# Performance work log

Measured on AMD Instinct MI355X. Metric: run time of the kernel, lower is better.

Reference implementation:

```python
import jax, jax.numpy as jnp
import numpy as np

N = 100000
E = 3200000
NFEAT = 512
NHID = 256
NCLASS = 40


def setup_inputs() -> dict:
    key = jax.random.key(0)
    k1, k2, k3, k4, k5 = jax.random.split(key, 5)
    x = jax.random.normal(k1, (N, NFEAT), dtype=jnp.float32)
    edge_index = jax.random.randint(k2, (2, E), 0, N, dtype=jnp.int64)
    edge_weight = jax.random.uniform(k3, (E,), dtype=jnp.float32)
    W1 = jax.random.normal(k4, (NFEAT, NHID), dtype=jnp.float32) / np.sqrt(NFEAT)
    b1 = jnp.zeros((NHID,), dtype=jnp.float32)
    W2 = jax.random.normal(k5, (NHID, NCLASS), dtype=jnp.float32) / np.sqrt(NHID)
    b2 = jnp.zeros((NCLASS,), dtype=jnp.float32)
    return {"x": x, "edge_index": edge_index, "edge_weight": edge_weight,
            "W1": W1, "b1": b1, "W2": W2, "b2": b2}


def reference(x, edge_index, edge_weight, W1, b1, W2, b2):
    rows = edge_index[0]  # destination nodes
    cols = edge_index[1]  # source nodes

    def spmm(h):
        # adj @ h via edge-list gather -> weight -> scatter-add  [N, d]
        return jax.ops.segment_sum(edge_weight[:, None] * h[cols], rows,
                                   num_segments=N)

    # baseline == 1 path of GCN.forward (dropout is identity in eval)
    h = jax.nn.relu(spmm(x @ W1 + b1))               # [N, NHID]
    logits = spmm(h @ W2 + b2)                       # [N, NCLASS]
    # original computes t.log(F.softmax(x, dim=1))
    return jnp.log(jax.nn.softmax(logits, axis=1))
```

## Files before the change

### kernel.cpp

```cpp
#include <hip/hip_runtime.h>
#include <hip/hip_fp16.h>
#include <math.h>

#define NNODES 100000
#define NEDGES 3200000
#define NFEAT  512
#define NHID   256
#define NCLASS 40
#define DPB    128
#define NBUCK  782
#define TILE   16384
#define NTILE  196

typedef _Float16 half8 __attribute__((ext_vector_type(8)));
typedef _Float16 half4 __attribute__((ext_vector_type(4)));
typedef float  f32x4  __attribute__((ext_vector_type(4)));

__global__ __launch_bounds__(256) void w1_f16_kernel(
    const float* __restrict__ W1, _Float16* __restrict__ W1T)
{
    const int i = blockIdx.x * 256 + threadIdx.x;
    if (i >= NFEAT * NHID) return;
    const int k = i >> 8;
    const int n = i & 255;
    W1T[n * NFEAT + k] = (_Float16)W1[i];
}

__global__ __launch_bounds__(256) void gemm1_f16_kernel(
    const float* __restrict__ x, const _Float16* __restrict__ Bt,
    const float* __restrict__ b1, _Float16* __restrict__ h0)
{
    __shared__ __align__(16) _Float16 As[64 * 40];
    const int t = threadIdx.x;
    const int lane = t & 63;
    const int w = t >> 6;
    const int row0 = blockIdx.x * 64;
    const int wn0 = w * 64;
    const int fr = lane & 15;
    const int fq = lane >> 4;
    const int srow = t >> 2;
    const int skq  = (t & 3) * 8;
    const int grow = row0 + srow;
    const float* xp = x + (size_t)grow * NFEAT + skq;
    _Float16* ap = &As[srow * 40 + skq];

    f32x4 acc[4][4] = {};

    for (int k0 = 0; k0 < NFEAT; k0 += 32) {
        half8 hv;
        if (grow < NNODES) {
            const float4 u0 = *(const float4*)(xp + k0);
            const float4 u1 = *(const float4*)(xp + k0 + 4);
            hv[0] = (_Float16)u0.x; hv[1] = (_Float16)u0.y;
            hv[2] = (_Float16)u0.z; hv[3] = (_Float16)u0.w;
            hv[4] = (_Float16)u1.x; hv[5] = (_Float16)u1.y;
            hv[6] = (_Float16)u1.z; hv[7] = (_Float16)u1.w;
        } else {
            #pragma unroll
            for (int j = 0; j < 8; ++j) hv[j] = (_Float16)0.f;
        }
        __syncthreads();
        *(half8*)ap = hv;
        __syncthreads();

        half8 a_f[4];
        #pragma unroll
        for (int mt = 0; mt < 4; ++mt)
            a_f[mt] = *(const half8*)&As[(mt * 16 + fr) * 40 + fq * 8];
        half8 b_f[4];
        #pragma unroll
        for (int nt = 0; nt < 4; ++nt) {
            const int n = wn0 + nt * 16 + fr;
            b_f[nt] = *(const half8*)(Bt + (size_t)n * NFEAT + k0 + fq * 8);
        }
        #pragma unroll
        for (int mt = 0; mt < 4; ++mt)
            #pragma unroll
            for (int nt = 0; nt < 4; ++nt)
                acc[mt][nt] = __builtin_amdgcn_mfma_f32_16x16x32_f16(
                    a_f[mt], b_f[nt], acc[mt][nt], 0, 0, 0);
    }
    #pragma unroll
    for (int mt = 0; mt < 4; ++mt)
        #pragma unroll
        for (int nt = 0; nt < 4; ++nt) {
            const int c = wn0 + nt * 16 + fr;
            const float bias = b1[c];
            const int r0 = row0 + mt * 16 + fq * 4;
            #pragma unroll
            for (int r = 0; r < 4; ++r) {
                const int row = r0 + r;
                if (row < NNODES)
                    h0[(size_t)row * NHID + c] = (_Float16)(acc[mt][nt][r] + bias);
            }
        }
}

__global__ __launch_bounds__(256) void gemm2_kernel(
    const float* __restrict__ h1, const float* __restrict__ W2,
    const float* __restrict__ b2, _Float16* __restrict__ h2)
{
    __shared__ float Bs[NHID * NCLASS];
    __shared__ float As[64][33];
    const int t = threadIdx.x;
    const int row0 = blockIdx.x * 64;
    for (int i = t; i < NHID * NCLASS; i += 256) Bs[i] = W2[i];
    const int r  = t & 63;
    const int cg = (t >> 6) * 10;
    const int am = t >> 2, ak = (t & 3) * 8;
    float acc[10] = {};
    for (int k0 = 0; k0 < NHID; k0 += 32) {
        __syncthreads();
        float4 v0 = make_float4(0.f,0.f,0.f,0.f), v1 = v0;
        const int arow = row0 + am;
        if (arow < NNODES) {
            v0 = *(const float4*)(h1 + (size_t)arow * NHID + k0 + ak);
            v1 = *(const float4*)(h1 + (size_t)arow * NHID + k0 + ak + 4);
        }
        As[am][ak + 0] = v0.x; As[am][ak + 1] = v0.y;
        As[am][ak + 2] = v0.z; As[am][ak + 3] = v0.w;
        As[am][ak + 4] = v1.x; As[am][ak + 5] = v1.y;
        As[am][ak + 6] = v1.z; As[am][ak + 7] = v1.w;
        __syncthreads();
        #pragma unroll
        for (int k = 0; k < 32; ++k) {
            const float a = As[r][k];
            #pragma unroll
            for (int j = 0; j < 10; ++j)
                acc[j] += a * Bs[(k0 + k) * NCLASS + cg + j];
        }
    }
    const int arow = row0 + r;
    if (arow < NNODES) {
        #pragma unroll
        for (int j = 0; j < 10; ++j)
            h2[(size_t)arow * NCLASS + cg + j] = (_Float16)(acc[j] + b2[cg + j]);
    }
}

__global__ __launch_bounds__(256) void csr_init_kernel(
    int* __restrict__ bhist, int* __restrict__ rowptr)
{
    const int i = blockIdx.x * 256 + threadIdx.x;
    if (i < NBUCK) bhist[i] = 0;
    if (i == 0) rowptr[NNODES] = NEDGES;
}

__global__ __launch_bounds__(256) void bin_count_kernel(
    const int* __restrict__ ei, int* __restrict__ bhist)
{
    __shared__ int h[NBUCK];
    const int t = threadIdx.x;
    for (int i = t; i < NBUCK; i += 256) h[i] = 0;
    __syncthreads();
    const int base = blockIdx.x * TILE;
    #pragma unroll 1
    for (int it = 0; it < TILE / 1024; ++it) {
        const int e = base + it * 1024 + t * 4;
        if (e + 3 < NEDGES) {
            const int4 d = *(const int4*)(ei + e);
            atomicAdd(&h[d.x >> 7], 1);
            atomicAdd(&h[d.y >> 7], 1);
            atomicAdd(&h[d.z >> 7], 1);
            atomicAdd(&h[d.w >> 7], 1);
        } else {
            for (int j = e; j < NEDGES; ++j) atomicAdd(&h[ei[j] >> 7], 1);
        }
    }
    __syncthreads();
    for (int i = t; i < NBUCK; i += 256)
        if (h[i]) atomicAdd(&bhist[i], h[i]);
}

__global__ __launch_bounds__(1024) void bucket_scan_kernel(
    const int* __restrict__ bhist, int* __restrict__ bbase, int* __restrict__ bcur)
{
    __shared__ int s[1024];
    const int t = threadIdx.x;
    const int v = (t < NBUCK) ? bhist[t] : 0;
    s[t] = v;
    __syncthreads();
    for (int o = 1; o < 1024; o <<= 1) {
        const int u = (t >= o) ? s[t - o] : 0;
        __syncthreads();
        s[t] += u;
        __syncthreads();
    }
    if (t < NBUCK) { bbase[t] = s[t] - v; bcur[t] = s[t] - v; }
    if (t == 1023) bbase[NBUCK] = s[1023];
}

__global__ __launch_bounds__(256) void bin_scatter_kernel(
    const int* __restrict__ ei, const float* __restrict__ ew,
    int* __restrict__ bcur, int2* __restrict__ binned)
{
    __shared__ int h[NBUCK];
    __shared__ int cur[NBUCK];
    const int t = threadIdx.x;
    for (int i = t; i < NBUCK; i += 256) h[i] = 0;
    __syncthreads();
    const int base = blockIdx.x * TILE;
    #pragma unroll 1
    for (int it = 0; it < TILE / 1024; ++it) {
        const int e = base + it * 1024 + t * 4;
        if (e + 3 < NEDGES) {
            const int4 d = *(const int4*)(ei + e);
            atomicAdd(&h[d.x >> 7], 1);
            atomicAdd(&h[d.y >> 7], 1);
            atomicAdd(&h[d.z >> 7], 1);
            atomicAdd(&h[d.w >> 7], 1);
        } else {
            for (int j = e; j < NEDGES; ++j) atomicAdd(&h[ei[j] >> 7], 1);
        }
    }
    __syncthreads();
    for (int i = t; i < NBUCK; i += 256)
        if (h[i]) cur[i] = atomicAdd(&bcur[i], h[i]);
    __syncthreads();
    #pragma unroll 1
    for (int it = 0; it < TILE / 1024; ++it) {
        const int e = base + it * 1024 + t * 4;
        if (e + 3 < NEDGES) {
            const int4   d = *(const int4*)(ei + e);
            const int4   s = *(const int4*)(ei + NEDGES + e);
            const float4 w = *(const float4*)(ew + e);
            int p0 = atomicAdd(&cur[d.x >> 7], 1);
            int p1 = atomicAdd(&cur[d.y >> 7], 1);
            int p2 = atomicAdd(&cur[d.z >> 7], 1);
            int p3 = atomicAdd(&cur[d.w >> 7], 1);
            binned[p0] = make_int2(((d.x & 127) << 17) | s.x, __float_as_int(w.x));
            binned[p1] = make_int2(((d.y & 127) << 17) | s.y, __float_as_int(w.y));
            binned[p2] = make_int2(((d.z & 127) << 17) | s.z, __float_as_int(w.z));
            binned[p3] = make_int2(((d.w & 127) << 17) | s.w, __float_as_int(w.w));
        } else {
            for (int j = e; j < NEDGES; ++j) {
                const int dj = ei[j];
                const int p = atomicAdd(&cur[dj >> 7], 1);
                binned[p] = make_int2(((dj & 127) << 17) | ei[NEDGES + j],
                                      __float_as_int(ew[j]));
            }
        }
    }
}

__global__ __launch_bounds__(256) void regroup_kernel(
    const int* __restrict__ bbase, const int2* __restrict__ binned,
    int* __restrict__ rowptr, int2* __restrict__ pairs)
{
    __shared__ int cnt[DPB];
    __shared__ int s[DPB];
    const int b = blockIdx.x;
    const int t = threadIdx.x;
    const int d0 = b * DPB;
    const int nd = (NNODES - d0 < DPB) ? (NNODES - d0) : DPB;
    if (t < DPB) cnt[t] = 0;
    __syncthreads();
    const int lo = bbase[b], hiE = bbase[b + 1];
    for (int idx = lo + t; idx < hiE; idx += 256)
        atomicAdd(&cnt[binned[idx].x >> 17], 1);
    __syncthreads();
    const int v = (t < DPB) ? cnt[t] : 0;
    if (t < DPB) s[t] = v;
    __syncthreads();
    for (int o = 1; o < DPB; o <<= 1) {
        const int u = (t >= o && t < DPB) ? s[t - o] : 0;
        __syncthreads();
        if (t < DPB) s[t] += u;
        __syncthreads();
    }
    if (t < nd) {
        const int base = lo + s[t] - v;
        rowptr[d0 + t] = base;
        cnt[t] = base;
    }
    __syncthreads();
    for (int idx = lo + t; idx < hiE; idx += 256) {
        const int2 e = binned[idx];
        const int l = e.x >> 17;
        const int pos = atomicAdd(&cnt[l], 1);
        pairs[pos] = make_int2(e.x & 0x1FFFF, e.y);
    }
}

__global__ __launch_bounds__(256) void spmm1_f16_kernel(
    const int* __restrict__ rowptr, const int2* __restrict__ pairs,
    const _Float16* __restrict__ h0, float* __restrict__ h1)
{
    const int dst  = blockIdx.x * 4 + (threadIdx.x >> 6);
    const int lane = threadIdx.x & 63;
    if (dst >= NNODES) return;
    const int beg = rowptr[dst], end = rowptr[dst + 1];
    const _Float16* base = h0 + lane * 4;
    float a0[4] = {0.f, 0.f, 0.f, 0.f};
    float a1[4] = {0.f, 0.f, 0.f, 0.f};
    int j = beg;
    for (; j + 1 < end; j += 2) {
        const int2 p0 = pairs[j];
        const int2 p1 = pairs[j + 1];
        const half4 v0 = *(const half4*)(base + (size_t)p0.x * NHID);
        const half4 v1 = *(const half4*)(base + (size_t)p1.x * NHID);
        const float w0 = __int_as_float(p0.y), w1 = __int_as_float(p1.y);
        #pragma unroll
        for (int k = 0; k < 4; ++k) {
            a0[k] = fmaf((float)v0[k], w0, a0[k]);
            a1[k] = fmaf((float)v1[k], w1, a1[k]);
        }
    }
    if (j < end) {
        const int2 p0 = pairs[j];
        const half4 v0 = *(const half4*)(base + (size_t)p0.x * NHID);
        const float w0 = __int_as_float(p0.y);
        #pragma unroll
        for (int k = 0; k < 4; ++k)
            a0[k] = fmaf((float)v0[k], w0, a0[k]);
    }
    float4 o;
    o.x = fmaxf(a0[0] + a1[0], 0.f);
    o.y = fmaxf(a0[1] + a1[1], 0.f);
    o.z = fmaxf(a0[2] + a1[2], 0.f);
    o.w = fmaxf(a0[3] + a1[3], 0.f);
    *(float4*)(h1 + (size_t)dst * NHID + lane * 4) = o;
}

__global__ __launch_bounds__(256) void spmm2_csr_kernel(
    const int* __restrict__ rowptr, const int2* __restrict__ pairs,
    const _Float16* __restrict__ h2, float* __restrict__ out)
{
    const int dst  = blockIdx.x * 4 + (threadIdx.x >> 6);
    const int lane = threadIdx.x & 63;
    if (dst >= NNODES) return;
    const int beg = rowptr[dst], end = rowptr[dst + 1];
    float a0 = 0.f, a1 = 0.f;
    int j = beg;
    for (; j + 1 < end; j += 2) {
        const int2 p0 = pairs[j];
        const int2 p1 = pairs[j + 1];
        float v0 = 0.f, v1 = 0.f;
        if (lane < NCLASS) {
            v0 = (float)h2[(size_t)p0.x * NCLASS + lane];
            v1 = (float)h2[(size_t)p1.x * NCLASS + lane];
        }
        a0 = fmaf(v0, __int_as_float(p0.y), a0);
        a1 = fmaf(v1, __int_as_float(p1.y), a1);
    }
    if (j < end) {
        const int2 p0 = pairs[j];
        float v0 = 0.f;
        if (lane < NCLASS) v0 = (float)h2[(size_t)p0.x * NCLASS + lane];
        a0 = fmaf(v0, __int_as_float(p0.y), a0);
    }
    const float acc = a0 + a1;
    float val = (lane < NCLASS) ? acc : -INFINITY;
    float m = val;
    #pragma unroll
    for (int o = 32; o >= 1; o >>= 1) m = fmaxf(m, __shfl_xor(m, o));
    float ex = (lane < NCLASS) ? expf(val - m) : 0.f;
    float s = ex;
    #pragma unroll
    for (int o = 32; o >= 1; o >>= 1) s += __shfl_xor(s, o);
    if (lane < NCLASS) out[(size_t)dst * NCLASS + lane] = val - m - logf(s);
}

extern "C" void kernel_launch(void* const* d_in, const int* in_sizes, int n_in,
                              void* d_out, int out_size, void* d_ws, size_t ws_size,
                              hipStream_t stream)
{
    const float* x  = (const float*)d_in[0];
    const int*   ei = (const int*)d_in[1];
    const float* ew = (const float*)d_in[2];
    const float* W1 = (const float*)d_in[3];
    const float* b1 = (const float*)d_in[4];
    const float* W2 = (const float*)d_in[5];
    const float* b2 = (const float*)d_in[6];
    float* out = (float*)d_out;

    char* ws = (char*)d_ws;
    const size_t H_BYTES = (size_t)NNODES * NHID * 4;
    _Float16* h0 = (_Float16*)(ws);
    float* h1 = (float*)(ws + H_BYTES);
    int2* binned = (int2*)(ws + H_BYTES);
    int2* pairs  = (int2*)(ws + 2 * H_BYTES);
    char* region = ws + 2 * H_BYTES + (size_t)NEDGES * 8;
    _Float16* W1T = (_Float16*)(region);
    int* rowptr = (int*)(region);
    int* bhist  = (int*)(region + 400016);
    int* bbase  = (int*)(region + 403152);
    int* bcur   = (int*)(region + 406288);
    _Float16* h2 = (_Float16*)(ws);

    w1_f16_kernel<<<(NFEAT * NHID + 255) / 256, 256, 0, stream>>>(W1, W1T);
    gemm1_f16_kernel<<<(NNODES + 63) / 64, 256, 0, stream>>>(x, W1T, b1, h0);
    csr_init_kernel<<<(NBUCK + 255) / 256, 256, 0, stream>>>(bhist, rowptr);
    bin_count_kernel<<<NTILE, 256, 0, stream>>>(ei, bhist);
    bucket_scan_kernel<<<1, 1024, 0, stream>>>(bhist, bbase, bcur);
    bin_scatter_kernel<<<NTILE, 256, 0, stream>>>(ei, ew, bcur, binned);
    regroup_kernel<<<NBUCK, 256, 0, stream>>>(bbase, binned, rowptr, pairs);
    spmm1_f16_kernel<<<(NNODES + 3) / 4, 256, 0, stream>>>(rowptr, pairs, h0, h1);
    gemm2_kernel<<<(NNODES + 63) / 64, 256, 0, stream>>>(h1, W2, b2, h2);
    spmm2_csr_kernel<<<(NNODES + 3) / 4, 256, 0, stream>>>(rowptr, pairs, h2, out);
}
```

Baseline: 713.3 us.

## Store hidden activations in fp16 and sub-sort CSR edges by source slice

The intermediate h1 produced by the first SpMM is now stored as fp16 instead of fp32, and gemm2 reads it as half8 vectors. This halves the write and read traffic for that buffer. Separately, the regroup kernel now sorts each destination's edges into 16 source-index slices using a larger shared-memory counting sort with a 256-wide scan. The goal is more locality in the SpMM gathers. Costs are reduced precision for h1 and extra scan work in regroup.

```diff
diff --git a/kernel.cpp b/kernel.cpp
--- a/kernel.cpp
+++ b/kernel.cpp
@@ -9,6 +9,7 @@
 #define NCLASS 40
 #define DPB    128
 #define NBUCK  782
+#define NSLICE 16
 #define TILE   16384
 #define NTILE  196
 
@@ -97,7 +98,7 @@
 }
 
 __global__ __launch_bounds__(256) void gemm2_kernel(
-    const float* __restrict__ h1, const float* __restrict__ W2,
+    const _Float16* __restrict__ h1, const float* __restrict__ W2,
     const float* __restrict__ b2, _Float16* __restrict__ h2)
 {
     __shared__ float Bs[NHID * NCLASS];
@@ -111,16 +112,15 @@
     float acc[10] = {};
     for (int k0 = 0; k0 < NHID; k0 += 32) {
         __syncthreads();
-        float4 v0 = make_float4(0.f,0.f,0.f,0.f), v1 = v0;
+        half8 hv;
+        #pragma unroll
+        for (int j = 0; j < 8; ++j) hv[j] = (_Float16)0.f;
         const int arow = row0 + am;
-        if (arow < NNODES) {
-            v0 = *(const float4*)(h1 + (size_t)arow * NHID + k0 + ak);
-            v1 = *(const float4*)(h1 + (size_t)arow * NHID + k0 + ak + 4);
-        }
-        As[am][ak + 0] = v0.x; As[am][ak + 1] = v0.y;
-        As[am][ak + 2] = v0.z; As[am][ak + 3] = v0.w;
-        As[am][ak + 4] = v1.x; As[am][ak + 5] = v1.y;
-        As[am][ak + 6] = v1.z; As[am][ak + 7] = v1.w;
+        if (arow < NNODES)
+            hv = *(const half8*)(h1 + (size_t)arow * NHID + k0 + ak);
+        #pragma unroll
+        for (int j = 0; j < 8; ++j)
+            As[am][ak + j] = (float)hv[j];
         __syncthreads();
         #pragma unroll
         for (int k = 0; k < 32; ++k) {
@@ -247,44 +247,58 @@
     const int* __restrict__ bbase, const int2* __restrict__ binned,
     int* __restrict__ rowptr, int2* __restrict__ pairs)
 {
-    __shared__ int cnt[DPB];
-    __shared__ int s[DPB];
+    __shared__ int cnt[DPB * NSLICE];
+    __shared__ int ss[256];
     const int b = blockIdx.x;
     const int t = threadIdx.x;
     const int d0 = b * DPB;
     const int nd = (NNODES - d0 < DPB) ? (NNODES - d0) : DPB;
-    if (t < DPB) cnt[t] = 0;
+    #pragma unroll
+    for (int j = 0; j < (DPB * NSLICE) / 256; ++j) cnt[j * 256 + t] = 0;
     __syncthreads();
     const int lo = bbase[b], hiE = bbase[b + 1];
-    for (int idx = lo + t; idx < hiE; idx += 256)
-        atomicAdd(&cnt[binned[idx].x >> 17], 1);
-    __syncthreads();
-    const int v = (t < DPB) ? cnt[t] : 0;
-    if (t < DPB) s[t] = v;
-    __syncthreads();
-    for (int o = 1; o < DPB; o <<= 1) {
-        const int u = (t >= o && t < DPB) ? s[t - o] : 0;
-        __syncthreads();
-        if (t < DPB) s[t] += u;
-        __syncthreads();
-    }
-    if (t < nd) {
-        const int base = lo + s[t] - v;
-        rowptr[d0 + t] = base;
-        cnt[t] = base;
+    for (int idx = lo + t; idx < hiE; idx += 256) {
+        const int xv = binned[idx].x;
+        const int key = ((xv >> 17) << 4) | ((xv & 0x1FFFF) >> 13);
+        atomicAdd(&cnt[key], 1);
+    }
+    __syncthreads();
+    int v[8];
+    int tsum = 0;
+    #pragma unroll
+    for (int j = 0; j < 8; ++j) { v[j] = cnt[8 * t + j]; tsum += v[j]; }
+    ss[t] = tsum;
+    __syncthreads();
+    for (int o = 1; o < 256; o <<= 1) {
+        const int u = (t >= o) ? ss[t - o] : 0;
+        __syncthreads();
+        ss[t] += u;
+        __syncthreads();
+    }
+    int run = lo + ss[t] - tsum;
+    #pragma unroll
+    for (int j = 0; j < 8; ++j) {
+        const int key = 8 * t + j;
+        cnt[key] = run;
+        if ((key & (NSLICE - 1)) == 0) {
+            const int d = key >> 4;
+            if (d < nd) rowptr[d0 + d] = run;
+        }
+        run += v[j];
     }
     __syncthreads();
     for (int idx = lo + t; idx < hiE; idx += 256) {
         const int2 e = binned[idx];
-        const int l = e.x >> 17;
-        const int pos = atomicAdd(&cnt[l], 1);
-        pairs[pos] = make_int2(e.x & 0x1FFFF, e.y);
+        const int src = e.x & 0x1FFFF;
+        const int key = ((e.x >> 17) << 4) | (src >> 13);
+        const int pos = atomicAdd(&cnt[key], 1);
+        pairs[pos] = make_int2(src, e.y);
     }
 }
 
 __global__ __launch_bounds__(256) void spmm1_f16_kernel(
     const int* __restrict__ rowptr, const int2* __restrict__ pairs,
-    const _Float16* __restrict__ h0, float* __restrict__ h1)
+    const _Float16* __restrict__ h0, _Float16* __restrict__ h1)
 {
     const int dst  = blockIdx.x * 4 + (threadIdx.x >> 6);
     const int lane = threadIdx.x & 63;
@@ -314,12 +328,12 @@
         for (int k = 0; k < 4; ++k)
             a0[k] = fmaf((float)v0[k], w0, a0[k]);
     }
-    float4 o;
-    o.x = fmaxf(a0[0] + a1[0], 0.f);
-    o.y = fmaxf(a0[1] + a1[1], 0.f);
-    o.z = fmaxf(a0[2] + a1[2], 0.f);
-    o.w = fmaxf(a0[3] + a1[3], 0.f);
-    *(float4*)(h1 + (size_t)dst * NHID + lane * 4) = o;
+    half4 o;
+    o[0] = (_Float16)fmaxf(a0[0] + a1[0], 0.f);
+    o[1] = (_Float16)fmaxf(a0[1] + a1[1], 0.f);
+    o[2] = (_Float16)fmaxf(a0[2] + a1[2], 0.f);
+    o[3] = (_Float16)fmaxf(a0[3] + a1[3], 0.f);
+    *(half4*)(h1 + (size_t)dst * NHID + lane * 4) = o;
 }
 
 __global__ __launch_bounds__(256) void spmm2_csr_kernel(
@@ -377,7 +391,7 @@
     char* ws = (char*)d_ws;
     const size_t H_BYTES = (size_t)NNODES * NHID * 4;
     _Float16* h0 = (_Float16*)(ws);
-    float* h1 = (float*)(ws + H_BYTES);
+    _Float16* h1 = (_Float16*)(ws + H_BYTES);
     int2* binned = (int2*)(ws + H_BYTES);
     int2* pairs  = (int2*)(ws + 2 * H_BYTES);
     char* region = ws + 2 * H_BYTES + (size_t)NEDGES * 8;
```

Measured after the change: 719.8 us. About the same (+0.9%).

## Store hidden activations in fp16 and enlarge gemm1 row tile to 128

Applied to the files above, without the earlier changes.

The ReLU output of the first SpMM is now written as fp16 instead of fp32, and gemm2 reads it as half8 and converts to float in shared memory. This halves the write and read traffic for the 100k x 256 intermediate. Separately, gemm1 now handles 128 rows per block with 8x4 MFMA accumulators, so each W1 fragment loaded from global memory is reused across twice as many rows. The cost is higher register pressure in gemm1, which may reduce occupancy, plus some extra rounding error in the hidden activations.

```diff
diff --git a/kernel.cpp b/kernel.cpp
--- a/kernel.cpp
+++ b/kernel.cpp
@@ -30,42 +30,49 @@
     const float* __restrict__ x, const _Float16* __restrict__ Bt,
     const float* __restrict__ b1, _Float16* __restrict__ h0)
 {
-    __shared__ __align__(16) _Float16 As[64 * 40];
+    __shared__ __align__(16) _Float16 As[128 * 40];
     const int t = threadIdx.x;
     const int lane = t & 63;
     const int w = t >> 6;
-    const int row0 = blockIdx.x * 64;
+    const int row0 = blockIdx.x * 128;
     const int wn0 = w * 64;
     const int fr = lane & 15;
     const int fq = lane >> 4;
-    const int srow = t >> 2;
-    const int skq  = (t & 3) * 8;
+    const int srow = t >> 1;
+    const int skq  = (t & 1) * 16;
     const int grow = row0 + srow;
     const float* xp = x + (size_t)grow * NFEAT + skq;
     _Float16* ap = &As[srow * 40 + skq];
 
-    f32x4 acc[4][4] = {};
+    f32x4 acc[8][4] = {};
 
     for (int k0 = 0; k0 < NFEAT; k0 += 32) {
-        half8 hv;
+        half8 hv0, hv1;
         if (grow < NNODES) {
             const float4 u0 = *(const float4*)(xp + k0);
             const float4 u1 = *(const float4*)(xp + k0 + 4);
-            hv[0] = (_Float16)u0.x; hv[1] = (_Float16)u0.y;
-            hv[2] = (_Float16)u0.z; hv[3] = (_Float16)u0.w;
-            hv[4] = (_Float16)u1.x; hv[5] = (_Float16)u1.y;
-            hv[6] = (_Float16)u1.z; hv[7] = (_Float16)u1.w;
+            const float4 u2 = *(const float4*)(xp + k0 + 8);
+            const float4 u3 = *(const float4*)(xp + k0 + 12);
+            hv0[0] = (_Float16)u0.x; hv0[1] = (_Float16)u0.y;
+            hv0[2] = (_Float16)u0.z; hv0[3] = (_Float16)u0.w;
+            hv0[4] = (_Float16)u1.x; hv0[5] = (_Float16)u1.y;
+            hv0[6] = (_Float16)u1.z; hv0[7] = (_Float16)u1.w;
+            hv1[0] = (_Float16)u2.x; hv1[1] = (_Float16)u2.y;
+            hv1[2] = (_Float16)u2.z; hv1[3] = (_Float16)u2.w;
+            hv1[4] = (_Float16)u3.x; hv1[5] = (_Float16)u3.y;
+            hv1[6] = (_Float16)u3.z; hv1[7] = (_Float16)u3.w;
         } else {
             #pragma unroll
-            for (int j = 0; j < 8; ++j) hv[j] = (_Float16)0.f;
-        }
-        __syncthreads();
-        *(half8*)ap = hv;
-        __syncthreads();
-
-        half8 a_f[4];
-        #pragma unroll
-        for (int mt = 0; mt < 4; ++mt)
+            for (int j = 0; j < 8; ++j) { hv0[j] = (_Float16)0.f; hv1[j] = (_Float16)0.f; }
+        }
+        __syncthreads();
+        *(half8*)ap = hv0;
+        *(half8*)(ap + 8) = hv1;
+        __syncthreads();
+
+        half8 a_f[8];
+        #pragma unroll
+        for (int mt = 0; mt < 8; ++mt)
             a_f[mt] = *(const half8*)&As[(mt * 16 + fr) * 40 + fq * 8];
         half8 b_f[4];
         #pragma unroll
@@ -74,14 +81,14 @@
             b_f[nt] = *(const half8*)(Bt + (size_t)n * NFEAT + k0 + fq * 8);
         }
         #pragma unroll
-        for (int mt = 0; mt < 4; ++mt)
+        for (int mt = 0; mt < 8; ++mt)
             #pragma unroll
             for (int nt = 0; nt < 4; ++nt)
                 acc[mt][nt] = __builtin_amdgcn_mfma_f32_16x16x32_f16(
                     a_f[mt], b_f[nt], acc[mt][nt], 0, 0, 0);
     }
     #pragma unroll
-    for (int mt = 0; mt < 4; ++mt)
+    for (int mt = 0; mt < 8; ++mt)
         #pragma unroll
         for (int nt = 0; nt < 4; ++nt) {
             const int c = wn0 + nt * 16 + fr;
@@ -97,7 +104,7 @@
 }
 
 __global__ __launch_bounds__(256) void gemm2_kernel(
-    const float* __restrict__ h1, const float* __restrict__ W2,
+    const _Float16* __restrict__ h1, const float* __restrict__ W2,
     const float* __restrict__ b2, _Float16* __restrict__ h2)
 {
     __shared__ float Bs[NHID * NCLASS];
@@ -111,16 +118,15 @@
     float acc[10] = {};
     for (int k0 = 0; k0 < NHID; k0 += 32) {
         __syncthreads();
-        float4 v0 = make_float4(0.f,0.f,0.f,0.f), v1 = v0;
+        half8 hv;
+        #pragma unroll
+        for (int j = 0; j < 8; ++j) hv[j] = (_Float16)0.f;
         const int arow = row0 + am;
-        if (arow < NNODES) {
-            v0 = *(const float4*)(h1 + (size_t)arow * NHID + k0 + ak);
-            v1 = *(const float4*)(h1 + (size_t)arow * NHID + k0 + ak + 4);
-        }
-        As[am][ak + 0] = v0.x; As[am][ak + 1] = v0.y;
-        As[am][ak + 2] = v0.z; As[am][ak + 3] = v0.w;
-        As[am][ak + 4] = v1.x; As[am][ak + 5] = v1.y;
-        As[am][ak + 6] = v1.z; As[am][ak + 7] = v1.w;
+        if (arow < NNODES)
+            hv = *(const half8*)(h1 + (size_t)arow * NHID + k0 + ak);
+        #pragma unroll
+        for (int j = 0; j < 8; ++j)
+            As[am][ak + j] = (float)hv[j];
         __syncthreads();
         #pragma unroll
         for (int k = 0; k < 32; ++k) {
@@ -284,7 +290,7 @@
 
 __global__ __launch_bounds__(256) void spmm1_f16_kernel(
     const int* __restrict__ rowptr, const int2* __restrict__ pairs,
-    const _Float16* __restrict__ h0, float* __restrict__ h1)
+    const _Float16* __restrict__ h0, _Float16* __restrict__ h1)
 {
     const int dst  = blockIdx.x * 4 + (threadIdx.x >> 6);
     const int lane = threadIdx.x & 63;
@@ -314,12 +320,12 @@
         for (int k = 0; k < 4; ++k)
             a0[k] = fmaf((float)v0[k], w0, a0[k]);
     }
-    float4 o;
-    o.x = fmaxf(a0[0] + a1[0], 0.f);
-    o.y = fmaxf(a0[1] + a1[1], 0.f);
-    o.z = fmaxf(a0[2] + a1[2], 0.f);
-    o.w = fmaxf(a0[3] + a1[3], 0.f);
-    *(float4*)(h1 + (size_t)dst * NHID + lane * 4) = o;
+    half4 o;
+    o[0] = (_Float16)fmaxf(a0[0] + a1[0], 0.f);
+    o[1] = (_Float16)fmaxf(a0[1] + a1[1], 0.f);
+    o[2] = (_Float16)fmaxf(a0[2] + a1[2], 0.f);
+    o[3] = (_Float16)fmaxf(a0[3] + a1[3], 0.f);
+    *(half4*)(h1 + (size_t)dst * NHID + lane * 4) = o;
 }
 
 __global__ __launch_bounds__(256) void spmm2_csr_kernel(
@@ -377,7 +383,7 @@
     char* ws = (char*)d_ws;
     const size_t H_BYTES = (size_t)NNODES * NHID * 4;
     _Float16* h0 = (_Float16*)(ws);
-    float* h1 = (float*)(ws + H_BYTES);
+    _Float16* h1 = (_Float16*)(ws + H_BYTES);
     int2* binned = (int2*)(ws + H_BYTES);
     int2* pairs  = (int2*)(ws + 2 * H_BYTES);
     char* region = ws + 2 * H_BYTES + (size_t)NEDGES * 8;
@@ -389,7 +395,7 @@
     _Float16* h2 = (_Float16*)(ws);
 
     w1_f16_kernel<<<(NFEAT * NHID + 255) / 256, 256, 0, stream>>>(W1, W1T);
-    gemm1_f16_kernel<<<(NNODES + 63) / 64, 256, 0, stream>>>(x, W1T, b1, h0);
+    gemm1_f16_kernel<<<(NNODES + 127) / 128, 256, 0, stream>>>(x, W1T, b1, h0);
     csr_init_kernel<<<(NBUCK + 255) / 256, 256, 0, stream>>>(bhist, rowptr);
     bin_count_kernel<<<NTILE, 256, 0, stream>>>(ei, bhist);
     bucket_scan_kernel<<<1, 1024, 0, stream>>>(bhist, bbase, bcur);
```

Result: slower. 741.5 us (+3.9%).
